# Kernel tuning notes

Hardware: AMD Instinct MI355X
Metric: run time of the kernel (lower is better)

The kernel has to match this reference:

```python
import jax, jax.numpy as jnp
import numpy as np
import math

NUM_HEADS = 8
CANTOR_DEPTH = 8
LOCAL_WINDOW = 16


def _cantor_routes(T, depth=CANTOR_DEPTH, window=LOCAL_WINDOW):
    # Vectorized Cantor coordinate per position, then top-k nearest neighbors.
    pos = jnp.arange(T, dtype=jnp.float32)
    x = jnp.clip(pos / max(1, T - 1), 1e-6, 1.0 - 1e-6)
    c = jnp.zeros_like(x)
    factor = 0.5
    for _ in range(depth):
        x = x * 3.0
        digit = jnp.floor(x)
        x = x - digit
        c = c + factor * (digit == 2.0).astype(jnp.float32)
        factor *= 0.5
    dist = jnp.abs(c[:, None] - c[None, :])  # [T, T]
    _, idx = jax.lax.top_k(-dist, min(window, T))  # smallest distances
    return idx  # [T, window] int32


def setup_inputs() -> dict:
    key = jax.random.key(0)
    ks = jax.random.split(key, 10)
    B, T, D = 2, 4096, 512
    s = 1.0 / math.sqrt(D)
    return {
        "x": jax.random.normal(ks[0], (B, T, D), dtype=jnp.float32),
        "Wq": jax.random.normal(ks[1], (D, D), dtype=jnp.float32) * s,
        "bq": jnp.zeros((D,), dtype=jnp.float32),
        "Wk": jax.random.normal(ks[2], (D, D), dtype=jnp.float32) * s,
        "bk": jnp.zeros((D,), dtype=jnp.float32),
        "Wv": jax.random.normal(ks[3], (D, D), dtype=jnp.float32) * s,
        "bv": jnp.zeros((D,), dtype=jnp.float32),
        "Wo": jax.random.normal(ks[4], (D, D), dtype=jnp.float32) * s,
        "bo": jnp.zeros((D,), dtype=jnp.float32),
        "temperature": jnp.float32(0.07),
    }


def reference(x, Wq, bq, Wk, bk, Wv, bv, Wo, bo, temperature):
    B, T, D = x.shape
    H = NUM_HEADS
    hd = D // H

    def proj(W, b):
        return (x @ W + b).reshape(B, T, H, hd).transpose(0, 2, 1, 3)  # [B,H,T,hd]

    Q = proj(Wq, bq)
    K = proj(Wk, bk)
    V = proj(Wv, bv)

    routes = _cantor_routes(T)  # [T, W]
    k_n = K[:, :, routes, :]  # [B,H,T,W,hd] gather of routed neighbors
    v_n = V[:, :, routes, :]

    scale = math.sqrt(hd) * jnp.abs(temperature)
    scores = jnp.einsum('bhtd,bhtwd->bhtw', Q, k_n) / scale
    attn = jax.nn.softmax(scores, axis=-1)
    out = jnp.einsum('bhtw,bhtwd->bhtd', attn, v_n)  # [B,H,T,hd]
    out = out.transpose(0, 2, 1, 3).reshape(B, T, D)
    return out @ Wo + bo
```

## Files before the change

### kernel.cpp

```cpp
#include <hip/hip_runtime.h>
#include <hip/hip_bf16.h>
#include <cstdint>
#include <climits>

#define TT 4096
#define DD 512
#define HH 8
#define HD 64
#define WW 16
#define CDEPTH 8

typedef unsigned short ushortT;
typedef unsigned int uintT;
using bf16x8 = __attribute__((ext_vector_type(8))) short;
using f32x4  = __attribute__((ext_vector_type(4))) float;

static __device__ __forceinline__ uintT f2bf(float v) {
    __hip_bfloat16 h = __float2bfloat16(v);
    return (uintT)*reinterpret_cast<ushortT*>(&h);
}
static __device__ __forceinline__ float bf2f(uintT u) {
    return __uint_as_float(u << 16);
}

static __device__ __forceinline__ int swz_idx(int r, int c) {
    const int u = r >> 1;
    const int s = (((r & 1) << 2) | c) ^ (u & 7);
    return (u << 6) + (s << 3);
}

static __device__ __forceinline__ int cantor_m(int t) {
    float x = (float)t / (float)(TT - 1);
    x = fminf(fmaxf(x, 1e-6f), 1.0f - 1e-6f);
    int m = 0;
    #pragma unroll
    for (int i = 0; i < CDEPTH; ++i) {
        float x3 = x * 3.0f;
        float dg = floorf(x3);
        x = x3 - dg;
        m = (m << 1) | ((dg == 2.0f) ? 1 : 0);
    }
    return m;
}

__global__ __launch_bounds__(256) void routes_f16_kernel(int* __restrict__ kv_g,
                                                         int* __restrict__ cnt_g,
                                                         int* __restrict__ f16_g) {
    __shared__ int kvloc[TT];
    __shared__ int pscan[256];
    const int tid = threadIdx.x;
    const int b = blockIdx.x;

    #pragma unroll
    for (int i = 0; i < 16; ++i) {
        const int t = i * 256 + tid;
        kvloc[t] = cantor_m(t);
    }
    __syncthreads();

    if (tid < 16) kv_g[b * 16 + tid] = kvloc[b * 16 + tid];

    int localcnt = 0;
    #pragma unroll
    for (int i = 0; i < 16; ++i)
        localcnt += (kvloc[tid * 16 + i] == b) ? 1 : 0;

    pscan[tid] = localcnt;
    __syncthreads();
    #pragma unroll
    for (int off = 1; off < 256; off <<= 1) {
        int v = (tid >= off) ? pscan[tid - off] : 0;
        __syncthreads();
        pscan[tid] += v;
        __syncthreads();
    }
    const int excl = pscan[tid] - localcnt;

    int r = excl;
    #pragma unroll
    for (int i = 0; i < 16; ++i) {
        const int t = tid * 16 + i;
        if (kvloc[t] == b) {
            if (r < 16) f16_g[b * 16 + r] = t;
            ++r;
        }
    }
    if (tid == 255) cnt_g[b] = pscan[255];
}

__global__ __launch_bounds__(256) void routes_merge_kernel(const int* __restrict__ cnt_g,
                                                           const int* __restrict__ f16_g,
                                                           int* __restrict__ table) {
    __shared__ int cnt[256];
    __shared__ int f16[256][16];
    const int tid = threadIdx.x;
    cnt[tid] = cnt_g[tid];
    {
        int4 a = reinterpret_cast<const int4*>(f16_g)[tid * 4 + 0];
        int4 b4 = reinterpret_cast<const int4*>(f16_g)[tid * 4 + 1];
        int4 c4 = reinterpret_cast<const int4*>(f16_g)[tid * 4 + 2];
        int4 d4 = reinterpret_cast<const int4*>(f16_g)[tid * 4 + 3];
        f16[tid][0] = a.x;  f16[tid][1] = a.y;  f16[tid][2] = a.z;  f16[tid][3] = a.w;
        f16[tid][4] = b4.x; f16[tid][5] = b4.y; f16[tid][6] = b4.z; f16[tid][7] = b4.w;
        f16[tid][8] = c4.x; f16[tid][9] = c4.y; f16[tid][10] = c4.z; f16[tid][11] = c4.w;
        f16[tid][12] = d4.x; f16[tid][13] = d4.y; f16[tid][14] = d4.z; f16[tid][15] = d4.w;
    }
    __syncthreads();

    int rtl[WW];
    int n = 0;
    {
        int c = cnt[tid];
        int take = (c < WW) ? c : WW;
        for (int i = 0; i < take; ++i) rtl[n++] = f16[tid][i];
    }
    for (int d = 1; n < WW && d <= 256; ++d) {
        const int lo = tid - d, hi = tid + d;
        const int clo = (lo >= 0) ? cnt[lo] : 0;
        const int chi = (hi < 256) ? cnt[hi] : 0;
        const int need = WW - n;
        if (clo + chi <= need) {
            for (int i = 0; i < clo; ++i) rtl[n++] = f16[lo][i];
            for (int i = 0; i < chi; ++i) rtl[n++] = f16[hi][i];
        } else {
            const int cl = (clo < WW) ? clo : WW;
            const int ch = (chi < WW) ? chi : WW;
            int i = 0, j = 0;
            while (n < WW) {
                int a = (i < cl) ? f16[lo][i] : INT_MAX;
                int b = (j < ch) ? f16[hi][j] : INT_MAX;
                if (a < b) { rtl[n++] = a; ++i; }
                else       { rtl[n++] = b; ++j; }
            }
        }
    }
    #pragma unroll
    for (int i = 0; i < WW; ++i) table[tid * WW + i] = rtl[i];
}

__global__ __launch_bounds__(256) void convw_split_kernel(
        const float* __restrict__ W0, const float* __restrict__ W1,
        const float* __restrict__ W2, const float* __restrict__ W3,
        ushortT* __restrict__ H0, ushortT* __restrict__ L0,
        ushortT* __restrict__ H1, ushortT* __restrict__ L1,
        ushortT* __restrict__ H2, ushortT* __restrict__ L2,
        ushortT* __restrict__ H3, ushortT* __restrict__ L3) {
    const float* src; ushortT* dh; ushortT* dl;
    switch (blockIdx.z) {
        case 0: src = W0; dh = H0; dl = L0; break;
        case 1: src = W1; dh = H1; dl = L1; break;
        case 2: src = W2; dh = H2; dl = L2; break;
        default: src = W3; dh = H3; dl = L3; break;
    }
    __shared__ float tile[32][33];
    const int k0 = blockIdx.y * 32, n0 = blockIdx.x * 32;
    const int ty = threadIdx.x >> 3;
    const int tx = (threadIdx.x & 7) * 4;
    const float4 v = *reinterpret_cast<const float4*>(&src[(size_t)(k0 + ty) * DD + n0 + tx]);
    tile[ty][tx + 0] = v.x; tile[ty][tx + 1] = v.y; tile[ty][tx + 2] = v.z; tile[ty][tx + 3] = v.w;
    __syncthreads();
    uintT rh[4], rl[4];
    #pragma unroll
    for (int j = 0; j < 4; ++j) {
        float f = tile[tx + j][ty];
        uintT h = f2bf(f);
        rh[j] = h;
        rl[j] = f2bf(f - bf2f(h));
    }
    uint2 oh, ol;
    oh.x = rh[0] | (rh[1] << 16); oh.y = rh[2] | (rh[3] << 16);
    ol.x = rl[0] | (rl[1] << 16); ol.y = rl[2] | (rl[3] << 16);
    *reinterpret_cast<uint2*>(&dh[(size_t)(n0 + ty) * DD + k0 + tx]) = oh;
    *reinterpret_cast<uint2*>(&dl[(size_t)(n0 + ty) * DD + k0 + tx]) = ol;
}

#define QBM 64
#define QBN 128
#define QBK 32
#define QKV_NWG 1536
#define OUT_NWG 512

__global__ __launch_bounds__(256, 6) void qkv_gemm(const float* __restrict__ x,
        const ushortT* __restrict__ Wqh, const ushortT* __restrict__ Wql,
        const ushortT* __restrict__ Wkh, const ushortT* __restrict__ Wkl,
        const ushortT* __restrict__ Wvh, const ushortT* __restrict__ Wvl,
        const float* __restrict__ bq, const float* __restrict__ bk, const float* __restrict__ bv,
        float* __restrict__ Qo, float* __restrict__ Ko, ushortT* __restrict__ Vo, int M) {
    __shared__ short Ash[QBM * QBK];
    __shared__ short Asl[QBM * QBK];
    __shared__ short Bsh[QBN * QBK];
    __shared__ short Bsl[QBN * QBK];
    const int tid = threadIdx.x;
    const int lane = tid & 63;
    const int wid = tid >> 6;

    const int id = blockIdx.x;
    const int swz = (id & 7) * (QKV_NWG / 8) + (id >> 3);
    const int bm = (swz / 12) * QBM;
    const int bnG = (swz % 12) * QBN;
    const int seg = bnG >> 9;
    const int bn = bnG & 511;
    const ushortT* __restrict__ Bhp = (seg == 0) ? Wqh : (seg == 1) ? Wkh : Wvh;
    const ushortT* __restrict__ Blp = (seg == 0) ? Wql : (seg == 1) ? Wkl : Wvl;
    const float* __restrict__ bias = (seg == 0) ? bq : (seg == 1) ? bk : bv;

    const int wr = wid >> 1;
    const int wc = wid & 1;

    f32x4 acc[2][4];
    #pragma unroll
    for (int i = 0; i < 2; ++i)
        #pragma unroll
        for (int j = 0; j < 4; ++j)
            acc[i][j] = (f32x4){0.f, 0.f, 0.f, 0.f};

    const int arow = tid >> 2;
    const int achk = tid & 3;
    const int fr = lane & 15;
    const int kq = lane >> 4;

    for (int k0 = 0; k0 < DD; k0 += QBK) {
        {
            const float* src = &x[(size_t)(bm + arow) * DD + k0 + achk * 8];
            const float4 v0 = *reinterpret_cast<const float4*>(src);
            const float4 v1 = *reinterpret_cast<const float4*>(src + 4);
            const float vv[8] = {v0.x, v0.y, v0.z, v0.w, v1.x, v1.y, v1.z, v1.w};
            bf16x8 vh, vl;
            #pragma unroll
            for (int j = 0; j < 8; ++j) {
                uintT h = f2bf(vv[j]);
                vh[j] = (short)h;
                vl[j] = (short)f2bf(vv[j] - bf2f(h));
            }
            const int ai = swz_idx(arow, achk);
            *reinterpret_cast<bf16x8*>(&Ash[ai]) = vh;
            *reinterpret_cast<bf16x8*>(&Asl[ai]) = vl;
        }
        #pragma unroll
        for (int s = 0; s < 2; ++s) {
            const int slot = tid + s * 256;
            const int br = slot >> 2;
            const int bchk = slot & 3;
            const size_t g = (size_t)(bn + br) * DD + k0 + bchk * 8;
            const int bi = swz_idx(br, bchk);
            *reinterpret_cast<bf16x8*>(&Bsh[bi]) = *reinterpret_cast<const bf16x8*>(&Bhp[g]);
            *reinterpret_cast<bf16x8*>(&Bsl[bi]) = *reinterpret_cast<const bf16x8*>(&Blp[g]);
        }
        __syncthreads();
        {
            bf16x8 avh[2], avl[2], bvh[4], bvl[4];
            #pragma unroll
            for (int i = 0; i < 2; ++i) {
                const int ai = swz_idx(wr * 32 + i * 16 + fr, kq);
                avh[i] = *reinterpret_cast<const bf16x8*>(&Ash[ai]);
                avl[i] = *reinterpret_cast<const bf16x8*>(&Asl[ai]);
            }
            #pragma unroll
            for (int j = 0; j < 4; ++j) {
                const int bi = swz_idx(wc * 64 + j * 16 + fr, kq);
                bvh[j] = *reinterpret_cast<const bf16x8*>(&Bsh[bi]);
                bvl[j] = *reinterpret_cast<const bf16x8*>(&Bsl[bi]);
            }
            #pragma unroll
            for (int i = 0; i < 2; ++i)
                #pragma unroll
                for (int j = 0; j < 4; ++j) {
                    acc[i][j] = __builtin_amdgcn_mfma_f32_16x16x32_bf16(avh[i], bvh[j], acc[i][j], 0, 0, 0);
                    acc[i][j] = __builtin_amdgcn_mfma_f32_16x16x32_bf16(avl[i], bvh[j], acc[i][j], 0, 0, 0);
                    acc[i][j] = __builtin_amdgcn_mfma_f32_16x16x32_bf16(avh[i], bvl[j], acc[i][j], 0, 0, 0);
                }
        }
        __syncthreads();
    }

    const int fq = lane >> 4;
    #pragma unroll
    for (int j = 0; j < 4; ++j) {
        const int col = bn + wc * 64 + j * 16 + fr;
        const float bvv = bias[col];
        #pragma unroll
        for (int i = 0; i < 2; ++i) {
            const int row0 = bm + wr * 32 + i * 16 + fq * 4;
            #pragma unroll
            for (int r = 0; r < 4; ++r) {
                const float val = acc[i][j][r] + bvv;
                if (seg == 2) {
                    Vo[(size_t)(row0 + r) * DD + col] = (ushortT)f2bf(val);
                } else {
                    float* dst = seg ? Ko : Qo;
                    dst[(size_t)(row0 + r) * DD + col] = val;
                }
            }
        }
    }
}

__global__ __launch_bounds__(256, 6) void out_gemm(const ushortT* __restrict__ Ahg,
                                                   const ushortT* __restrict__ Alg,
                                                   const ushortT* __restrict__ Bh,
                                                   const ushortT* __restrict__ Bl,
                                                   const float* __restrict__ bias,
                                                   float* __restrict__ C, int M) {
    __shared__ short Ash[QBM * QBK];
    __shared__ short Asl[QBM * QBK];
    __shared__ short Bsh[QBN * QBK];
    __shared__ short Bsl[QBN * QBK];
    const int tid = threadIdx.x;
    const int lane = tid & 63;
    const int wid = tid >> 6;

    const int id = blockIdx.x;
    const int swz = (id & 7) * (OUT_NWG / 8) + (id >> 3);
    const int bm = (swz >> 2) * QBM;
    const int bn = (swz & 3) * QBN;
    const int wr = wid >> 1;
    const int wc = wid & 1;

    f32x4 acc[2][4];
    #pragma unroll
    for (int i = 0; i < 2; ++i)
        #pragma unroll
        for (int j = 0; j < 4; ++j)
            acc[i][j] = (f32x4){0.f, 0.f, 0.f, 0.f};

    const int arow = tid >> 2;
    const int achk = tid & 3;
    const int fr = lane & 15;
    const int kq = lane >> 4;

    for (int k0 = 0; k0 < DD; k0 += QBK) {
        {
            const size_t g = (size_t)(bm + arow) * DD + k0 + achk * 8;
            const int ai = swz_idx(arow, achk);
            *reinterpret_cast<bf16x8*>(&Ash[ai]) = *reinterpret_cast<const bf16x8*>(&Ahg[g]);
            *reinterpret_cast<bf16x8*>(&Asl[ai]) = *reinterpret_cast<const bf16x8*>(&Alg[g]);
        }
        #pragma unroll
        for (int s = 0; s < 2; ++s) {
            const int slot = tid + s * 256;
            const int br = slot >> 2;
            const int bchk = slot & 3;
            const size_t g = (size_t)(bn + br) * DD + k0 + bchk * 8;
            const int bi = swz_idx(br, bchk);
            *reinterpret_cast<bf16x8*>(&Bsh[bi]) = *reinterpret_cast<const bf16x8*>(&Bh[g]);
            *reinterpret_cast<bf16x8*>(&Bsl[bi]) = *reinterpret_cast<const bf16x8*>(&Bl[g]);
        }
        __syncthreads();
        {
            bf16x8 avh[2], avl[2], bvh[4], bvl[4];
            #pragma unroll
            for (int i = 0; i < 2; ++i) {
                const int ai = swz_idx(wr * 32 + i * 16 + fr, kq);
                avh[i] = *reinterpret_cast<const bf16x8*>(&Ash[ai]);
                avl[i] = *reinterpret_cast<const bf16x8*>(&Asl[ai]);
            }
            #pragma unroll
            for (int j = 0; j < 4; ++j) {
                const int bi = swz_idx(wc * 64 + j * 16 + fr, kq);
                bvh[j] = *reinterpret_cast<const bf16x8*>(&Bsh[bi]);
                bvl[j] = *reinterpret_cast<const bf16x8*>(&Bsl[bi]);
            }
            #pragma unroll
            for (int i = 0; i < 2; ++i)
                #pragma unroll
                for (int j = 0; j < 4; ++j) {
                    acc[i][j] = __builtin_amdgcn_mfma_f32_16x16x32_bf16(avh[i], bvh[j], acc[i][j], 0, 0, 0);
                    acc[i][j] = __builtin_amdgcn_mfma_f32_16x16x32_bf16(avl[i], bvh[j], acc[i][j], 0, 0, 0);
                    acc[i][j] = __builtin_amdgcn_mfma_f32_16x16x32_bf16(avh[i], bvl[j], acc[i][j], 0, 0, 0);
                }
        }
        __syncthreads();
    }

    const int fq = lane >> 4;
    #pragma unroll
    for (int j = 0; j < 4; ++j) {
        const int col = bn + wc * 64 + j * 16 + fr;
        const float bvv = bias[col];
        #pragma unroll
        for (int i = 0; i < 2; ++i) {
            const int row0 = bm + wr * 32 + i * 16 + fq * 4;
            #pragma unroll
            for (int r = 0; r < 4; ++r)
                C[(size_t)(row0 + r) * DD + col] = acc[i][j][r] + bvv;
        }
    }
}

__global__ __launch_bounds__(256) void attn2_kernel(const float* __restrict__ Q,
                                                    const float* __restrict__ K,
                                                    const ushortT* __restrict__ V,
                                                    const int* __restrict__ kv_g,
                                                    const int* __restrict__ table,
                                                    const float* __restrict__ temp_ptr,
                                                    ushortT* __restrict__ AOh,
                                                    ushortT* __restrict__ AOl, int B) {
    const int lane = threadIdx.x & 63;
    const int u = (blockIdx.x * blockDim.x + threadIdx.x) >> 6;
    if (u >= B * TT) return;
    const int t = u & (TT - 1);
    const float scale_inv = 1.0f / (8.0f * fabsf(temp_ptr[0]));

    const int* rt = &table[kv_g[t] * WW];
    int sidx[WW];
    #pragma unroll
    for (int w = 0; w < WW; ++w) sidx[w] = rt[w];

    const size_t rowbase = (size_t)u * DD + lane * 8;
    const size_t bbase = (size_t)(u - t) * DD;
    const float4 q0 = *reinterpret_cast<const float4*>(&Q[rowbase]);
    const float4 q1 = *reinterpret_cast<const float4*>(&Q[rowbase + 4]);

    float sc[WW];
    #pragma unroll
    for (int w = 0; w < WW; ++w) {
        const float* kr = &K[bbase + (size_t)sidx[w] * DD + lane * 8];
        const float4 k0 = *reinterpret_cast<const float4*>(kr);
        const float4 k1 = *reinterpret_cast<const float4*>(kr + 4);
        float p = q0.x * k0.x + q0.y * k0.y + q0.z * k0.z + q0.w * k0.w
                + q1.x * k1.x + q1.y * k1.y + q1.z * k1.z + q1.w * k1.w;
        p += __shfl_xor(p, 1);
        p += __shfl_xor(p, 2);
        p += __shfl_xor(p, 4);
        sc[w] = p * scale_inv;
    }

    float m = sc[0];
    #pragma unroll
    for (int w = 1; w < WW; ++w) m = fmaxf(m, sc[w]);
    float pr[WW];
    float sum = 0.0f;
    #pragma unroll
    for (int w = 0; w < WW; ++w) { pr[w] = expf(sc[w] - m); sum += pr[w]; }
    const float inv = 1.0f / sum;

    float o[8] = {0.f, 0.f, 0.f, 0.f, 0.f, 0.f, 0.f, 0.f};
    #pragma unroll
    for (int w = 0; w < WW; ++w) {
        const uint4 vv = *reinterpret_cast<const uint4*>(&V[bbase + (size_t)sidx[w] * DD + lane * 8]);
        o[0] += pr[w] * bf2f(vv.x & 0xffffu); o[1] += pr[w] * bf2f(vv.x >> 16);
        o[2] += pr[w] * bf2f(vv.y & 0xffffu); o[3] += pr[w] * bf2f(vv.y >> 16);
        o[4] += pr[w] * bf2f(vv.z & 0xffffu); o[5] += pr[w] * bf2f(vv.z >> 16);
        o[6] += pr[w] * bf2f(vv.w & 0xffffu); o[7] += pr[w] * bf2f(vv.w >> 16);
    }
    uintT rh[8], rl[8];
    #pragma unroll
    for (int i = 0; i < 8; ++i) {
        const float val = o[i] * inv;
        uintT h = f2bf(val);
        rh[i] = h;
        rl[i] = f2bf(val - bf2f(h));
    }
    uint4 oh, ol;
    oh.x = rh[0] | (rh[1] << 16); oh.y = rh[2] | (rh[3] << 16);
    oh.z = rh[4] | (rh[5] << 16); oh.w = rh[6] | (rh[7] << 16);
    ol.x = rl[0] | (rl[1] << 16); ol.y = rl[2] | (rl[3] << 16);
    ol.z = rl[4] | (rl[5] << 16); ol.w = rl[6] | (rl[7] << 16);
    *reinterpret_cast<uint4*>(&AOh[rowbase]) = oh;
    *reinterpret_cast<uint4*>(&AOl[rowbase]) = ol;
}

extern "C" void kernel_launch(void* const* d_in, const int* in_sizes, int n_in,
                              void* d_out, int out_size, void* d_ws, size_t ws_size,
                              hipStream_t stream) {
    const float* x    = (const float*)d_in[0];
    const float* Wq   = (const float*)d_in[1];
    const float* bq   = (const float*)d_in[2];
    const float* Wk   = (const float*)d_in[3];
    const float* bk   = (const float*)d_in[4];
    const float* Wv   = (const float*)d_in[5];
    const float* bv   = (const float*)d_in[6];
    const float* Wo   = (const float*)d_in[7];
    const float* bo   = (const float*)d_in[8];
    const float* temp = (const float*)d_in[9];
    float* out = (float*)d_out;

    const int B = in_sizes[0] / (TT * DD);
    const int M = B * TT;
    const size_t MD = (size_t)M * DD;

    float* Qb = (float*)d_ws;
    float* Kb = Qb + MD;
    ushortT* Vb = (ushortT*)(Kb + MD);
    ushortT* AOh = Vb + MD;
    ushortT* AOl = AOh + MD;
    ushortT* Wqh = AOl + MD;
    ushortT* Wql = Wqh + DD * DD;
    ushortT* Wkh = Wql + DD * DD;
    ushortT* Wkl = Wkh + DD * DD;
    ushortT* Wvh = Wkl + DD * DD;
    ushortT* Wvl = Wvh + DD * DD;
    ushortT* Woh = Wvl + DD * DD;
    ushortT* Wol = Woh + DD * DD;
    int* kvg   = (int*)(Wol + DD * DD);
    int* table = kvg + TT;
    int* cntg  = table + 256 * WW;
    int* f16g  = cntg + 256;

    routes_f16_kernel<<<256, 256, 0, stream>>>(kvg, cntg, f16g);
    routes_merge_kernel<<<1, 256, 0, stream>>>(cntg, f16g, table);
    convw_split_kernel<<<dim3(16, 16, 4), 256, 0, stream>>>(Wq, Wk, Wv, Wo,
                                                            Wqh, Wql, Wkh, Wkl,
                                                            Wvh, Wvl, Woh, Wol);

    qkv_gemm<<<QKV_NWG, 256, 0, stream>>>(x, Wqh, Wql, Wkh, Wkl, Wvh, Wvl,
                                          bq, bk, bv, Qb, Kb, Vb, M);

    attn2_kernel<<<(M * 64) / 256, 256, 0, stream>>>(Qb, Kb, Vb, kvg, table, temp, AOh, AOl, B);

    out_gemm<<<OUT_NWG, 256, 0, stream>>>(AOh, AOl, Woh, Wol, bo, out, M);
}
```

Baseline: 158.1 us.

## Pre-tile weights in swizzled LDS layout and load B via global_load_lds

The weight conversion kernel now writes the split bf16 hi/lo weights into per-tile blocks already arranged in the GEMM's swizzled shared-memory layout. Both GEMMs then fill their B tiles with direct global-to-LDS loads, bypassing registers and the per-thread address arithmetic. The aim is to cut VGPR traffic and the instruction cost of staging B. In exchange, the conversion kernel reads the fp32 weights with strided, uncoalesced accesses, and correctness now depends on the global_load_lds lane-to-address mapping matching the swizzle.

```diff
diff --git a/kernel.cpp b/kernel.cpp
--- a/kernel.cpp
+++ b/kernel.cpp
@@ -28,6 +28,17 @@
     const int s = (((r & 1) << 2) | c) ^ (u & 7);
     return (u << 6) + (s << 3);
 }
+static __device__ __forceinline__ void inv_swz(int p, int& r, int& c) {
+    const int u = p >> 3;
+    const int bits = (p & 7) ^ (u & 7);
+    r = (u << 1) | (bits >> 2);
+    c = bits & 3;
+}
+
+#define GLDS(gsrc, ldst)                                                          \
+    __builtin_amdgcn_global_load_lds(                                             \
+        (const __attribute__((address_space(1))) uint32_t*)(gsrc),                \
+        (__attribute__((address_space(3))) uint32_t*)(ldst), 16, 0, 0)
 
 static __device__ __forceinline__ int cantor_m(int t) {
     float x = (float)t / (float)(TT - 1);
@@ -138,7 +149,7 @@
     for (int i = 0; i < WW; ++i) table[tid * WW + i] = rtl[i];
 }
 
-__global__ __launch_bounds__(256) void convw_split_kernel(
+__global__ __launch_bounds__(256) void convw_tile_kernel(
         const float* __restrict__ W0, const float* __restrict__ W1,
         const float* __restrict__ W2, const float* __restrict__ W3,
         ushortT* __restrict__ H0, ushortT* __restrict__ L0,
@@ -152,26 +163,33 @@
         case 2: src = W2; dh = H2; dl = L2; break;
         default: src = W3; dh = H3; dl = L3; break;
     }
-    __shared__ float tile[32][33];
-    const int k0 = blockIdx.y * 32, n0 = blockIdx.x * 32;
-    const int ty = threadIdx.x >> 3;
-    const int tx = (threadIdx.x & 7) * 4;
-    const float4 v = *reinterpret_cast<const float4*>(&src[(size_t)(k0 + ty) * DD + n0 + tx]);
-    tile[ty][tx + 0] = v.x; tile[ty][tx + 1] = v.y; tile[ty][tx + 2] = v.z; tile[ty][tx + 3] = v.w;
-    __syncthreads();
-    uintT rh[4], rl[4];
-    #pragma unroll
-    for (int j = 0; j < 4; ++j) {
-        float f = tile[tx + j][ty];
-        uintT h = f2bf(f);
-        rh[j] = h;
-        rl[j] = f2bf(f - bf2f(h));
-    }
-    uint2 oh, ol;
-    oh.x = rh[0] | (rh[1] << 16); oh.y = rh[2] | (rh[3] << 16);
-    ol.x = rl[0] | (rl[1] << 16); ol.y = rl[2] | (rl[3] << 16);
-    *reinterpret_cast<uint2*>(&dh[(size_t)(n0 + ty) * DD + k0 + tx]) = oh;
-    *reinterpret_cast<uint2*>(&dl[(size_t)(n0 + ty) * DD + k0 + tx]) = ol;
+    const int nt = blockIdx.x;
+    const int kt = blockIdx.y;
+    const size_t tilebase = ((size_t)(nt * 16 + kt)) * 4096;
+
+    #pragma unroll
+    for (int s = 0; s < 2; ++s) {
+        const int p = threadIdx.x + s * 256;
+        int r, c;
+        inv_swz(p, r, c);
+        const int n = nt * 128 + r;
+        const int k = kt * 32 + c * 8;
+        uintT rh[8], rl[8];
+        #pragma unroll
+        for (int j = 0; j < 8; ++j) {
+            const float f = src[(size_t)(k + j) * DD + n];
+            const uintT h = f2bf(f);
+            rh[j] = h;
+            rl[j] = f2bf(f - bf2f(h));
+        }
+        uint4 oh, ol;
+        oh.x = rh[0] | (rh[1] << 16); oh.y = rh[2] | (rh[3] << 16);
+        oh.z = rh[4] | (rh[5] << 16); oh.w = rh[6] | (rh[7] << 16);
+        ol.x = rl[0] | (rl[1] << 16); ol.y = rl[2] | (rl[3] << 16);
+        ol.z = rl[4] | (rl[5] << 16); ol.w = rl[6] | (rl[7] << 16);
+        *reinterpret_cast<uint4*>(&dh[tilebase + (size_t)p * 8]) = oh;
+        *reinterpret_cast<uint4*>(&dl[tilebase + (size_t)p * 8]) = ol;
+    }
 }
 
 #define QBM 64
@@ -218,12 +236,23 @@
     const int achk = tid & 3;
     const int fr = lane & 15;
     const int kq = lane >> 4;
+    const int nt = bn >> 7;
 
     for (int k0 = 0; k0 < DD; k0 += QBK) {
         {
-            const float* src = &x[(size_t)(bm + arow) * DD + k0 + achk * 8];
-            const float4 v0 = *reinterpret_cast<const float4*>(src);
-            const float4 v1 = *reinterpret_cast<const float4*>(src + 4);
+            const size_t tb = ((size_t)(nt * 16 + (k0 >> 5))) * 4096;
+            const int base = wid * 128;
+            #pragma unroll
+            for (int q = 0; q < 2; ++q) {
+                const size_t so = tb + (size_t)(base + q * 64 + lane) * 8;
+                GLDS(&Bhp[so], &Bsh[(base + q * 64) * 8]);
+                GLDS(&Blp[so], &Bsl[(base + q * 64) * 8]);
+            }
+        }
+        {
+            const float* srcp = &x[(size_t)(bm + arow) * DD + k0 + achk * 8];
+            const float4 v0 = *reinterpret_cast<const float4*>(srcp);
+            const float4 v1 = *reinterpret_cast<const float4*>(srcp + 4);
             const float vv[8] = {v0.x, v0.y, v0.z, v0.w, v1.x, v1.y, v1.z, v1.w};
             bf16x8 vh, vl;
             #pragma unroll
@@ -235,16 +264,6 @@
             const int ai = swz_idx(arow, achk);
             *reinterpret_cast<bf16x8*>(&Ash[ai]) = vh;
             *reinterpret_cast<bf16x8*>(&Asl[ai]) = vl;
-        }
-        #pragma unroll
-        for (int s = 0; s < 2; ++s) {
-            const int slot = tid + s * 256;
-            const int br = slot >> 2;
-            const int bchk = slot & 3;
-            const size_t g = (size_t)(bn + br) * DD + k0 + bchk * 8;
-            const int bi = swz_idx(br, bchk);
-            *reinterpret_cast<bf16x8*>(&Bsh[bi]) = *reinterpret_cast<const bf16x8*>(&Bhp[g]);
-            *reinterpret_cast<bf16x8*>(&Bsl[bi]) = *reinterpret_cast<const bf16x8*>(&Blp[g]);
         }
         __syncthreads();
         {
@@ -327,23 +346,24 @@
     const int achk = tid & 3;
     const int fr = lane & 15;
     const int kq = lane >> 4;
+    const int nt = bn >> 7;
 
     for (int k0 = 0; k0 < DD; k0 += QBK) {
+        {
+            const size_t tb = ((size_t)(nt * 16 + (k0 >> 5))) * 4096;
+            const int base = wid * 128;
+            #pragma unroll
+            for (int q = 0; q < 2; ++q) {
+                const size_t so = tb + (size_t)(base + q * 64 + lane) * 8;
+                GLDS(&Bh[so], &Bsh[(base + q * 64) * 8]);
+                GLDS(&Bl[so], &Bsl[(base + q * 64) * 8]);
+            }
+        }
         {
             const size_t g = (size_t)(bm + arow) * DD + k0 + achk * 8;
             const int ai = swz_idx(arow, achk);
             *reinterpret_cast<bf16x8*>(&Ash[ai]) = *reinterpret_cast<const bf16x8*>(&Ahg[g]);
             *reinterpret_cast<bf16x8*>(&Asl[ai]) = *reinterpret_cast<const bf16x8*>(&Alg[g]);
-        }
-        #pragma unroll
-        for (int s = 0; s < 2; ++s) {
-            const int slot = tid + s * 256;
-            const int br = slot >> 2;
-            const int bchk = slot & 3;
-            const size_t g = (size_t)(bn + br) * DD + k0 + bchk * 8;
-            const int bi = swz_idx(br, bchk);
-            *reinterpret_cast<bf16x8*>(&Bsh[bi]) = *reinterpret_cast<const bf16x8*>(&Bh[g]);
-            *reinterpret_cast<bf16x8*>(&Bsl[bi]) = *reinterpret_cast<const bf16x8*>(&Bl[g]);
         }
         __syncthreads();
         {
@@ -499,9 +519,9 @@
 
     routes_f16_kernel<<<256, 256, 0, stream>>>(kvg, cntg, f16g);
     routes_merge_kernel<<<1, 256, 0, stream>>>(cntg, f16g, table);
-    convw_split_kernel<<<dim3(16, 16, 4), 256, 0, stream>>>(Wq, Wk, Wv, Wo,
-                                                            Wqh, Wql, Wkh, Wkl,
-                                                            Wvh, Wvl, Woh, Wol);
+    convw_tile_kernel<<<dim3(4, 16, 4), 256, 0, stream>>>(Wq, Wk, Wv, Wo,
+                                                          Wqh, Wql, Wkh, Wkl,
+                                                          Wvh, Wvl, Woh, Wol);
 
     qkv_gemm<<<QKV_NWG, 256, 0, stream>>>(x, Wqh, Wql, Wkh, Wkl, Wvh, Wvl,
                                           bq, bk, bv, Qb, Kb, Vb, M);
```

Result: faster. 142.6 us (median of 12 runs) (-9.8%).
